# Optimization experiments

Hardware: AMD Instinct MI355X
Metric: run time of the kernel (lower is better)

## Reference

```python
import jax, jax.numpy as jnp
import numpy as np

B, Q, D, H, HD, LP, M = 16, 1, 2048, 16, 128, 2048, 8192
EPS = 1e-5

def _ln(x, w, b):
    mu = jnp.mean(x, axis=-1, keepdims=True)
    var = jnp.mean((x - mu) ** 2, axis=-1, keepdims=True)
    return (x - mu) * jax.lax.rsqrt(var + EPS) * w + b

def setup_inputs() -> dict:
    key = jax.random.key(0)
    ks = jax.random.split(key, 8)
    std = 0.02
    return {
        "input": jax.random.normal(ks[0], (B, Q, D), jnp.float32),
        "past_key": jax.random.normal(ks[1], (B, LP, H, HD), jnp.float32),
        "past_value": jax.random.normal(ks[2], (B, LP, H, HD), jnp.float32),
        "ln0_w": jnp.ones((D,), jnp.float32),
        "ln0_b": jnp.zeros((D,), jnp.float32),
        "ln1_w": jnp.ones((D,), jnp.float32),
        "ln1_b": jnp.zeros((D,), jnp.float32),
        "wqkv": jax.random.normal(ks[3], (3 * D, D), jnp.float32) * std,
        "wo": jax.random.normal(ks[4], (D, D), jnp.float32) * std,
        "fc0_w": jax.random.normal(ks[5], (M, D), jnp.float32) * std,
        "fc0_b": jnp.zeros((M,), jnp.float32),
        "fc1_w": jax.random.normal(ks[6], (D, M), jnp.float32) * std,
        "fc1_b": jnp.zeros((D,), jnp.float32),
    }

def reference(input, past_key, past_value, ln0_w, ln0_b, ln1_w, ln1_b,
              wqkv, wo, fc0_w, fc0_b, fc1_w, fc1_b):
    # norm0 + fused QKV projection (no bias)
    x = _ln(input, ln0_w, ln0_b)                       # [B,Q,D]
    qkv = (x @ wqkv.T).reshape(B, Q, 3, H, HD)
    q, k, v = qkv[:, :, 0], qkv[:, :, 1], qkv[:, :, 2]  # each [B,Q,H,HD]
    # append to KV cache
    k = jnp.concatenate([past_key, k], axis=1)          # [B,LP+Q,H,HD]
    v = jnp.concatenate([past_value, v], axis=1)
    # decode attention; q_len == 1 so no causal mask is applied (matches source)
    scores = jnp.einsum('nqhd,nkhd->nhqk', q, k) / (HD ** 0.5)
    attn = jax.nn.softmax(scores.astype(jnp.float32), axis=-1).astype(scores.dtype)
    attn_out = jnp.einsum('nhql,nlhd->nqhd', attn, v).reshape(B, Q, D)
    attn_out = attn_out @ wo.T
    h = input + attn_out
    # MLP2 with exact (erf) GELU as in torch F.gelu
    y = _ln(h, ln1_w, ln1_b)
    y = jax.nn.gelu(y @ fc0_w.T + fc0_b, approximate=False) @ fc1_w.T + fc1_b
    return h + y
```

## Files before the change

kernel.cpp:

```cpp
#include <hip/hip_runtime.h>
#include <math.h>

typedef __attribute__((ext_vector_type(4))) float f32x4;
typedef __attribute__((ext_vector_type(4))) _Float16 f16x4;

#define B_  16
#define D_  2048
#define H_  16
#define HD_ 128
#define LP_ 2048
#define M_  8192
#define QKV_R (3 * D_)
#define SCALE 0.08838834764831845f

__device__ inline float wave_sum(float v) {
  for (int m = 32; m > 0; m >>= 1) v += __shfl_xor(v, m);
  return v;
}
__device__ inline float wave_max(float v) {
  for (int m = 32; m > 0; m >>= 1) v = fmaxf(v, __shfl_xor(v, m));
  return v;
}

__global__ void ln_kernel(const float* __restrict__ x, const float* __restrict__ w,
                          const float* __restrict__ bb, float* __restrict__ o) {
  __shared__ float sred[4];
  int b = blockIdx.x, t = threadIdx.x;
  const float* xr = x + (size_t)b * D_;
  f32x4 v0 = *(const f32x4*)(xr + t * 8);
  f32x4 v1 = *(const f32x4*)(xr + t * 8 + 4);
  float s = (v0[0] + v0[1] + v0[2] + v0[3]) + (v1[0] + v1[1] + v1[2] + v1[3]);
  s = wave_sum(s);
  if ((t & 63) == 0) sred[t >> 6] = s;
  __syncthreads();
  float mu = (sred[0] + sred[1] + sred[2] + sred[3]) * (1.0f / D_);
  __syncthreads();
  float sq = 0.f;
  for (int i = 0; i < 4; i++) {
    float d0 = v0[i] - mu; sq += d0 * d0;
    float d1 = v1[i] - mu; sq += d1 * d1;
  }
  sq = wave_sum(sq);
  if ((t & 63) == 0) sred[t >> 6] = sq;
  __syncthreads();
  float var = (sred[0] + sred[1] + sred[2] + sred[3]) * (1.0f / D_);
  float rs = rsqrtf(var + 1e-5f);
  f32x4 w0 = *(const f32x4*)(w + t * 8), w1 = *(const f32x4*)(w + t * 8 + 4);
  f32x4 c0 = *(const f32x4*)(bb + t * 8), c1 = *(const f32x4*)(bb + t * 8 + 4);
  f32x4 o0, o1;
  for (int i = 0; i < 4; i++) {
    o0[i] = (v0[i] - mu) * rs * w0[i] + c0[i];
    o1[i] = (v1[i] - mu) * rs * w1[i] + c1[i];
  }
  *(f32x4*)(o + (size_t)b * D_ + t * 8) = o0;
  *(f32x4*)(o + (size_t)b * D_ + t * 8 + 4) = o1;
}

__global__ void gemv_k(const float* __restrict__ W, const float* __restrict__ X,
                       float* __restrict__ part, int R, int K, int kc) {
  int wave = threadIdx.x >> 6, lane = threadIdx.x & 63;
  int j0 = (blockIdx.x * 4 + wave) * 16;
  int k0 = blockIdx.y * kc;
  int col = lane & 15;
  int kg  = (lane >> 4) << 2;
  const float* wp = W + (size_t)(j0 + col) * K + k0 + kg;
  const float* xp = X + (size_t)col * K + k0 + kg;
  f32x4 acc = {0.f, 0.f, 0.f, 0.f};
  #pragma unroll 4
  for (int kk = 0; kk < kc; kk += 16) {
    f32x4 av = *(const f32x4*)xp; xp += 16;
    f32x4 bv = *(const f32x4*)wp; wp += 16;
    f16x4 ah, bh;
    for (int i = 0; i < 4; i++) { ah[i] = (_Float16)av[i]; bh[i] = (_Float16)bv[i]; }
    acc = __builtin_amdgcn_mfma_f32_16x16x16f16(ah, bh, acc, 0, 0, 0);
  }
  *(f32x4*)(part + ((size_t)blockIdx.y * R + j0 + col) * 16 + kg) = acc;
}

__global__ void reduce_plain(const float* __restrict__ part, float* __restrict__ out,
                             int R, int S) {
  int i = blockIdx.x * 256 + threadIdx.x;
  int j = i >> 4, b = i & 15;
  float s = 0.f;
  for (int k = 0; k < S; k++) s += part[(size_t)k * R * 16 + i];
  out[(size_t)b * R + j] = s;
}
__global__ void reduce_resid(const float* __restrict__ part, const float* __restrict__ resid,
                             float* __restrict__ out, int R, int S) {
  int i = blockIdx.x * 256 + threadIdx.x;
  int j = i >> 4, b = i & 15;
  float s = 0.f;
  for (int k = 0; k < S; k++) s += part[(size_t)k * R * 16 + i];
  out[(size_t)b * R + j] = resid[(size_t)b * R + j] + s;
}
__global__ void reduce_bias_gelu(const float* __restrict__ part, const float* __restrict__ bias,
                                 float* __restrict__ out, int R, int S) {
  int i = blockIdx.x * 256 + threadIdx.x;
  int j = i >> 4, b = i & 15;
  float s = 0.f;
  for (int k = 0; k < S; k++) s += part[(size_t)k * R * 16 + i];
  float u = s + bias[j];
  out[(size_t)b * R + j] = 0.5f * u * (1.0f + erff(u * 0.70710678118654752f));
}
__global__ void reduce_bias_resid(const float* __restrict__ part, const float* __restrict__ bias,
                                  const float* __restrict__ resid, float* __restrict__ out,
                                  int R, int S) {
  int i = blockIdx.x * 256 + threadIdx.x;
  int j = i >> 4, b = i & 15;
  float s = 0.f;
  for (int k = 0; k < S; k++) s += part[(size_t)k * R * 16 + i];
  out[(size_t)b * R + j] = resid[(size_t)b * R + j] + s + bias[j];
}

__global__ void attn_part(const float* __restrict__ qkv, const float* __restrict__ pk,
                          const float* __restrict__ pv, float* __restrict__ pml,
                          float* __restrict__ pacc) {
  int bh = blockIdx.x, split = blockIdx.y;
  int b = bh >> 4, hh = bh & 15;
  int t = threadIdx.x;
  __shared__ f32x4 q_s4[32];
  __shared__ float s_s[128];
  __shared__ float sred[4];
  __shared__ f32x4 redv[8][32];
  if (t < 128) ((float*)q_s4)[t] = qkv[(size_t)b * QKV_R + hh * HD_ + t] * SCALE;
  __syncthreads();
  int l0 = split * 128;
  int lane32 = t & 31, g = t >> 5;
  const float* kbase = pk + (((size_t)b * LP_ + l0) * H_ + hh) * HD_ + lane32 * 4;
  f32x4 qv = q_s4[lane32];
  for (int it = 0; it < 16; it++) {
    int kk = g * 16 + it;
    f32x4 kv = *(const f32x4*)(kbase + (size_t)kk * (H_ * HD_));
    float d = kv[0] * qv[0] + kv[1] * qv[1] + kv[2] * qv[2] + kv[3] * qv[3];
    for (int m = 16; m > 0; m >>= 1) d += __shfl_xor(d, m);
    if (lane32 == 0) s_s[kk] = d;
  }
  __syncthreads();
  float v = (t < 128) ? s_s[t] : -1e30f;
  float mw = wave_max(v);
  if ((t & 63) == 0) sred[t >> 6] = mw;
  __syncthreads();
  float M = fmaxf(fmaxf(sred[0], sred[1]), fmaxf(sred[2], sred[3]));
  __syncthreads();
  float p = (t < 128) ? __expf(v - M) : 0.f;
  float sw = wave_sum(p);
  if ((t & 63) == 0) sred[t >> 6] = sw;
  __syncthreads();
  float L = sred[0] + sred[1] + sred[2] + sred[3];
  if (t < 128) s_s[t] = p;
  if (t == 0) {
    pml[(bh * 16 + split) * 2]     = M;
    pml[(bh * 16 + split) * 2 + 1] = L;
  }
  __syncthreads();
  const float* vbase = pv + (((size_t)b * LP_ + l0) * H_ + hh) * HD_ + lane32 * 4;
  f32x4 acc = {0.f, 0.f, 0.f, 0.f};
  for (int it = 0; it < 16; it++) {
    int kk = g * 16 + it;
    f32x4 vv = *(const f32x4*)(vbase + (size_t)kk * (H_ * HD_));
    float pp = s_s[kk];
    for (int i = 0; i < 4; i++) acc[i] += pp * vv[i];
  }
  redv[g][lane32] = acc;
  __syncthreads();
  if (t < 32) {
    f32x4 o = redv[0][t];
    for (int g2 = 1; g2 < 8; g2++) {
      f32x4 r = redv[g2][t];
      for (int i = 0; i < 4; i++) o[i] += r[i];
    }
    *(f32x4*)(pacc + (size_t)(bh * 16 + split) * HD_ + t * 4) = o;
  }
}

__global__ void attn_comb(const float* __restrict__ qkv, const float* __restrict__ pml,
                          const float* __restrict__ pacc, float* __restrict__ attn_out) {
  int bh = blockIdx.x, b = bh >> 4, hh = bh & 15;
  int t = threadIdx.x;
  __shared__ float sred[2];
  float qv = qkv[(size_t)b * QKV_R + hh * HD_ + t];
  float kn = qkv[(size_t)b * QKV_R + D_ + hh * HD_ + t];
  float d = qv * kn;
  d = wave_sum(d);
  if ((t & 63) == 0) sred[t >> 6] = d;
  __syncthreads();
  float s_new = (sred[0] + sred[1]) * SCALE;
  float vn = qkv[(size_t)b * QKV_R + 2 * D_ + hh * HD_ + t];
  float M = s_new;
  for (int s = 0; s < 16; s++) M = fmaxf(M, pml[(bh * 16 + s) * 2]);
  float en = __expf(s_new - M);
  float L = en;
  float o = en * vn;
  for (int s = 0; s < 16; s++) {
    float ms = pml[(bh * 16 + s) * 2], ls = pml[(bh * 16 + s) * 2 + 1];
    float e = __expf(ms - M);
    L += ls * e;
    o += pacc[(size_t)(bh * 16 + s) * HD_ + t] * e;
  }
  attn_out[(size_t)b * D_ + hh * HD_ + t] = o / L;
}

extern "C" void kernel_launch(void* const* d_in, const int* in_sizes, int n_in,
                              void* d_out, int out_size, void* d_ws, size_t ws_size,
                              hipStream_t stream) {
  const float* input  = (const float*)d_in[0];
  const float* pk     = (const float*)d_in[1];
  const float* pv     = (const float*)d_in[2];
  const float* ln0_w  = (const float*)d_in[3];
  const float* ln0_b  = (const float*)d_in[4];
  const float* ln1_w  = (const float*)d_in[5];
  const float* ln1_b  = (const float*)d_in[6];
  const float* wqkv   = (const float*)d_in[7];
  const float* wo     = (const float*)d_in[8];
  const float* fc0_w  = (const float*)d_in[9];
  const float* fc0_b  = (const float*)d_in[10];
  const float* fc1_w  = (const float*)d_in[11];
  const float* fc1_b  = (const float*)d_in[12];
  float* out = (float*)d_out;

  char* wsb = (char*)d_ws;
  float* x_ln     = (float*)(wsb + 0);
  float* qkv      = (float*)(wsb + 131072);
  float* attn_out = (float*)(wsb + 524288);
  float* hbuf     = (float*)(wsb + 655360);
  float* y0       = (float*)(wsb + 786432);
  float* act      = (float*)(wsb + 917504);
  float* pml      = (float*)(wsb + 1441792);
  float* pacc     = (float*)(wsb + 1474560);
  float* part     = (float*)(wsb + 3571712);

  ln_kernel<<<16, 256, 0, stream>>>(input, ln0_w, ln0_b, x_ln);
  gemv_k<<<dim3(96, 8), 256, 0, stream>>>(wqkv, x_ln, part, QKV_R, D_, 256);
  reduce_plain<<<384, 256, 0, stream>>>(part, qkv, QKV_R, 8);
  attn_part<<<dim3(256, 16), 256, 0, stream>>>(qkv, pk, pv, pml, pacc);
  attn_comb<<<256, 128, 0, stream>>>(qkv, pml, pacc, attn_out);
  gemv_k<<<dim3(32, 16), 256, 0, stream>>>(wo, attn_out, part, D_, D_, 128);
  reduce_resid<<<128, 256, 0, stream>>>(part, input, hbuf, D_, 16);
  ln_kernel<<<16, 256, 0, stream>>>(hbuf, ln1_w, ln1_b, y0);
  gemv_k<<<dim3(128, 4), 256, 0, stream>>>(fc0_w, y0, part, M_, D_, 512);
  reduce_bias_gelu<<<512, 256, 0, stream>>>(part, fc0_b, act, M_, 4);
  gemv_k<<<dim3(32, 16), 256, 0, stream>>>(fc1_w, act, part, D_, M_, 512);
  reduce_bias_resid<<<128, 256, 0, stream>>>(part, fc1_b, hbuf, out, D_, 16);
}
```

Measured before the change: 204.8 us.

## Restructure decode attention so each block handles all heads of a contiguous KV chunk

Result: faster. 197.4 us (-3.6%).

```diff
diff --git a/kernel.cpp b/kernel.cpp
--- a/kernel.cpp
+++ b/kernel.cpp
@@ -12,13 +12,11 @@
 #define M_  8192
 #define QKV_R (3 * D_)
 #define SCALE 0.08838834764831845f
+#define NSPLIT 32
+#define KPS 64
 
 __device__ inline float wave_sum(float v) {
   for (int m = 32; m > 0; m >>= 1) v += __shfl_xor(v, m);
-  return v;
-}
-__device__ inline float wave_max(float v) {
-  for (int m = 32; m > 0; m >>= 1) v = fmaxf(v, __shfl_xor(v, m));
   return v;
 }
 
@@ -115,62 +113,57 @@
 __global__ void attn_part(const float* __restrict__ qkv, const float* __restrict__ pk,
                           const float* __restrict__ pv, float* __restrict__ pml,
                           float* __restrict__ pacc) {
-  int bh = blockIdx.x, split = blockIdx.y;
-  int b = bh >> 4, hh = bh & 15;
+  int b = blockIdx.x, split = blockIdx.y;
   int t = threadIdx.x;
-  __shared__ f32x4 q_s4[32];
-  __shared__ float s_s[128];
-  __shared__ float sred[4];
-  __shared__ f32x4 redv[8][32];
-  if (t < 128) ((float*)q_s4)[t] = qkv[(size_t)b * QKV_R + hh * HD_ + t] * SCALE;
-  __syncthreads();
-  int l0 = split * 128;
-  int lane32 = t & 31, g = t >> 5;
-  const float* kbase = pk + (((size_t)b * LP_ + l0) * H_ + hh) * HD_ + lane32 * 4;
-  f32x4 qv = q_s4[lane32];
-  for (int it = 0; it < 16; it++) {
-    int kk = g * 16 + it;
-    f32x4 kv = *(const f32x4*)(kbase + (size_t)kk * (H_ * HD_));
-    float d = kv[0] * qv[0] + kv[1] * qv[1] + kv[2] * qv[2] + kv[3] * qv[3];
-    for (int m = 16; m > 0; m >>= 1) d += __shfl_xor(d, m);
-    if (lane32 == 0) s_s[kk] = d;
-  }
-  __syncthreads();
-  float v = (t < 128) ? s_s[t] : -1e30f;
-  float mw = wave_max(v);
-  if ((t & 63) == 0) sred[t >> 6] = mw;
-  __syncthreads();
-  float M = fmaxf(fmaxf(sred[0], sred[1]), fmaxf(sred[2], sred[3]));
-  __syncthreads();
-  float p = (t < 128) ? __expf(v - M) : 0.f;
-  float sw = wave_sum(p);
-  if ((t & 63) == 0) sred[t >> 6] = sw;
-  __syncthreads();
-  float L = sred[0] + sred[1] + sred[2] + sred[3];
-  if (t < 128) s_s[t] = p;
-  if (t == 0) {
-    pml[(bh * 16 + split) * 2]     = M;
-    pml[(bh * 16 + split) * 2 + 1] = L;
-  }
-  __syncthreads();
-  const float* vbase = pv + (((size_t)b * LP_ + l0) * H_ + hh) * HD_ + lane32 * 4;
-  f32x4 acc = {0.f, 0.f, 0.f, 0.f};
-  for (int it = 0; it < 16; it++) {
-    int kk = g * 16 + it;
-    f32x4 vv = *(const f32x4*)(vbase + (size_t)kk * (H_ * HD_));
-    float pp = s_s[kk];
-    for (int i = 0; i < 4; i++) acc[i] += pp * vv[i];
-  }
-  redv[g][lane32] = acc;
-  __syncthreads();
-  if (t < 32) {
-    f32x4 o = redv[0][t];
-    for (int g2 = 1; g2 < 8; g2++) {
-      f32x4 r = redv[g2][t];
-      for (int i = 0; i < 4; i++) o[i] += r[i];
-    }
-    *(f32x4*)(pacc + (size_t)(bh * 16 + split) * HD_ + t * 4) = o;
-  }
+  int h = t >> 4, d0 = (t & 15) * 8;
+  __shared__ float s_s[16][KPS + 1];
+
+  f32x4 q0 = *(const f32x4*)(qkv + (size_t)b * QKV_R + h * HD_ + d0);
+  f32x4 q1 = *(const f32x4*)(qkv + (size_t)b * QKV_R + h * HD_ + d0 + 4);
+  for (int i = 0; i < 4; i++) { q0[i] *= SCALE; q1[i] *= SCALE; }
+
+  const float* kb = pk + ((size_t)b * LP_ + split * KPS) * D_ + t * 8;
+  #pragma unroll 4
+  for (int l = 0; l < KPS; l++) {
+    f32x4 k0 = *(const f32x4*)(kb + (size_t)l * D_);
+    f32x4 k1 = *(const f32x4*)(kb + (size_t)l * D_ + 4);
+    float d = q0[0]*k0[0] + q0[1]*k0[1] + q0[2]*k0[2] + q0[3]*k0[3]
+            + q1[0]*k1[0] + q1[1]*k1[1] + q1[2]*k1[2] + q1[3]*k1[3];
+    d += __shfl_xor(d, 1); d += __shfl_xor(d, 2);
+    d += __shfl_xor(d, 4); d += __shfl_xor(d, 8);
+    if ((t & 15) == 0) s_s[h][l] = d;
+  }
+  __syncthreads();
+
+  int l0 = (t & 15) * 4;
+  float sv0 = s_s[h][l0], sv1 = s_s[h][l0 + 1], sv2 = s_s[h][l0 + 2], sv3 = s_s[h][l0 + 3];
+  float m = fmaxf(fmaxf(sv0, sv1), fmaxf(sv2, sv3));
+  m = fmaxf(m, __shfl_xor(m, 1)); m = fmaxf(m, __shfl_xor(m, 2));
+  m = fmaxf(m, __shfl_xor(m, 4)); m = fmaxf(m, __shfl_xor(m, 8));
+  sv0 = __expf(sv0 - m); sv1 = __expf(sv1 - m);
+  sv2 = __expf(sv2 - m); sv3 = __expf(sv3 - m);
+  float L = sv0 + sv1 + sv2 + sv3;
+  L += __shfl_xor(L, 1); L += __shfl_xor(L, 2);
+  L += __shfl_xor(L, 4); L += __shfl_xor(L, 8);
+  s_s[h][l0] = sv0; s_s[h][l0 + 1] = sv1; s_s[h][l0 + 2] = sv2; s_s[h][l0 + 3] = sv3;
+  if ((t & 15) == 0) {
+    pml[((b * NSPLIT + split) * H_ + h) * 2]     = m;
+    pml[((b * NSPLIT + split) * H_ + h) * 2 + 1] = L;
+  }
+  __syncthreads();
+
+  const float* vb = pv + ((size_t)b * LP_ + split * KPS) * D_ + t * 8;
+  f32x4 a0 = {0.f, 0.f, 0.f, 0.f}, a1 = {0.f, 0.f, 0.f, 0.f};
+  #pragma unroll 4
+  for (int l = 0; l < KPS; l++) {
+    f32x4 v0 = *(const f32x4*)(vb + (size_t)l * D_);
+    f32x4 v1 = *(const f32x4*)(vb + (size_t)l * D_ + 4);
+    float p = s_s[h][l];
+    for (int i = 0; i < 4; i++) { a0[i] += p * v0[i]; a1[i] += p * v1[i]; }
+  }
+  size_t oi = (((size_t)b * NSPLIT + split) * H_ + h) * HD_ + d0;
+  *(f32x4*)(pacc + oi) = a0;
+  *(f32x4*)(pacc + oi + 4) = a1;
 }
 
 __global__ void attn_comb(const float* __restrict__ qkv, const float* __restrict__ pml,
@@ -187,15 +180,17 @@
   float s_new = (sred[0] + sred[1]) * SCALE;
   float vn = qkv[(size_t)b * QKV_R + 2 * D_ + hh * HD_ + t];
   float M = s_new;
-  for (int s = 0; s < 16; s++) M = fmaxf(M, pml[(bh * 16 + s) * 2]);
+  for (int s = 0; s < NSPLIT; s++)
+    M = fmaxf(M, pml[((b * NSPLIT + s) * H_ + hh) * 2]);
   float en = __expf(s_new - M);
   float L = en;
   float o = en * vn;
-  for (int s = 0; s < 16; s++) {
-    float ms = pml[(bh * 16 + s) * 2], ls = pml[(bh * 16 + s) * 2 + 1];
+  for (int s = 0; s < NSPLIT; s++) {
+    float ms = pml[((b * NSPLIT + s) * H_ + hh) * 2];
+    float ls = pml[((b * NSPLIT + s) * H_ + hh) * 2 + 1];
     float e = __expf(ms - M);
     L += ls * e;
-    o += pacc[(size_t)(bh * 16 + s) * HD_ + t] * e;
+    o += pacc[(((size_t)b * NSPLIT + s) * H_ + hh) * HD_ + t] * e;
   }
   attn_out[(size_t)b * D_ + hh * HD_ + t] = o / L;
 }
@@ -226,13 +221,13 @@
   float* y0       = (float*)(wsb + 786432);
   float* act      = (float*)(wsb + 917504);
   float* pml      = (float*)(wsb + 1441792);
-  float* pacc     = (float*)(wsb + 1474560);
-  float* part     = (float*)(wsb + 3571712);
+  float* pacc     = (float*)(wsb + 1507328);
+  float* part     = (float*)(wsb + 5701632);
 
   ln_kernel<<<16, 256, 0, stream>>>(input, ln0_w, ln0_b, x_ln);
   gemv_k<<<dim3(96, 8), 256, 0, stream>>>(wqkv, x_ln, part, QKV_R, D_, 256);
   reduce_plain<<<384, 256, 0, stream>>>(part, qkv, QKV_R, 8);
-  attn_part<<<dim3(256, 16), 256, 0, stream>>>(qkv, pk, pv, pml, pacc);
+  attn_part<<<dim3(B_, NSPLIT), 256, 0, stream>>>(qkv, pk, pv, pml, pacc);
   attn_comb<<<256, 128, 0, stream>>>(qkv, pml, pacc, attn_out);
   gemv_k<<<dim3(32, 16), 256, 0, stream>>>(wo, attn_out, part, D_, D_, 128);
   reduce_resid<<<128, 256, 0, stream>>>(part, input, hbuf, D_, 16);
```
